# Kernel tuning notes

Hardware: AMD Instinct MI355X
Metric: run time of the kernel (lower is better)

Reference implementation:

```python
import jax, jax.numpy as jnp
import numpy as np

# Model/config dims
U, B, D, H, R, S, M = 512, 16, 512, 8, 32, 16, 32
HD = D // H
Q = R + U + S          # query length
KV = M + R + U         # key/value length
PE = 2 * U - 1         # relative position embedding length (training mode)
NEG_INF = -1e8
SCALE = HD ** -0.5


def setup_inputs() -> dict:
    key = jax.random.key(0)
    ks = jax.random.split(key, 14)
    f = lambda k, shp: jax.random.normal(k, shp, dtype=jnp.float32)
    return {
        "utterance": f(ks[0], (U, B, D)),
        "lengths": jax.random.randint(ks[1], (B,), U // 2, U + 1),
        "right_context": f(ks[2], (R, B, D)),
        "summary": f(ks[3], (S, B, D)),
        "memory": f(ks[4], (M, B, D)),
        "attention_mask": jax.random.bernoulli(ks[5], 0.5, (Q, KV)),  # True = masked
        "pos_emb": f(ks[6], (PE, D)),
        "Wq": f(ks[7], (D, D)) * 0.02, "bq": jnp.zeros((D,), jnp.float32),
        "Wkv": f(ks[8], (2 * D, D)) * 0.02, "bkv": jnp.zeros((2 * D,), jnp.float32),
        "Wo": f(ks[9], (D, D)) * 0.02, "bo": jnp.zeros((D,), jnp.float32),
        "Wpos": f(ks[10], (D, D)) * 0.02,
        "pos_bias_u": f(ks[11], (H, HD)) * 0.02,
        "pos_bias_v": f(ks[12], (H, HD)) * 0.02,
    }


def _rel_shift(x):
    # x: (B, H, U, PE) -> (B, H, U, PE - U + 1); out[..., u, j] = x[..., u, (U-1) - u + j]
    b, h, u, pe = x.shape
    out_len = pe - (u - 1)
    idx = (u - 1) - jnp.arange(u)[:, None] + jnp.arange(out_len)[None, :]  # (U, out_len)
    return jnp.take_along_axis(x, idx[None, None], axis=3)


def reference(utterance, lengths, right_context, summary, memory, attention_mask,
              pos_emb, Wq, bq, Wkv, bkv, Wo, bo, Wpos, pos_bias_u, pos_bias_v):
    # Projections
    query = jnp.concatenate([right_context, utterance, summary]) @ Wq.T + bq      # (Q, B, D)
    kv = jnp.concatenate([memory, right_context, utterance]) @ Wkv.T + bkv        # (KV, B, 2D)
    key_t, val_t = jnp.split(kv, 2, axis=2)                                       # (KV, B, D) each

    rk = key_t.reshape(KV, B * H, HD).transpose(1, 0, 2)                          # (B*H, KV, HD)
    rv = val_t.reshape(KV, B * H, HD).transpose(1, 0, 2)
    q4 = query.reshape(Q, B, H, HD)

    # content term (matrix AC) with pos_bias_u
    qu = (q4 + pos_bias_u).reshape(Q, B * H, HD).transpose(1, 0, 2)               # (B*H, Q, HD)
    matrix_ac = jnp.einsum('nqd,nkd->nqk', qu, rk)                                # (B*H, Q, KV)

    # positional term (matrix BD) with pos_bias_v, only for utterance queries
    uv = (q4[R:R + U] + pos_bias_v).transpose(1, 2, 0, 3)                         # (B, H, U, HD)
    pos = (pos_emb @ Wpos.T).reshape(PE, H, HD).transpose(1, 0, 2)                # (H, PE, HD)
    bd = jnp.einsum('bhud,hpd->bhup', uv, pos)                                    # (B, H, U, PE)
    bd = _rel_shift(bd).reshape(B * H, U, -1)                                     # (B*H, U, U)
    matrix_bd = jnp.zeros_like(matrix_ac).at[:, R:R + U, M + R:].set(bd)

    w = (matrix_ac + matrix_bd) * SCALE
    w = jnp.where(attention_mask[None], NEG_INF, w)
    # padding mask (B > 1 branch): pad positions where kv index >= KV - U + lengths
    pad = jnp.arange(KV)[None, :] >= (KV - U + lengths)[:, None]                  # (B, KV)
    w = jnp.where(pad[:, None, None, :], NEG_INF, w.reshape(B, H, Q, KV)).reshape(B * H, Q, KV)

    probs = jax.nn.softmax(w, axis=-1)
    attn = jnp.einsum('nqk,nkd->nqd', probs, rv)                                  # (B*H, Q, HD)
    attn = attn.transpose(1, 0, 2).reshape(Q, B, D)
    outputs = attn @ Wo.T + bo

    out_right_context_utterance = outputs[:R + U]                                 # (R+U, B, D)
    out_memory = jnp.clip(outputs[R + U:], -10.0, 10.0)                           # (S, B, D), tanh_on_mem=False
    return out_right_context_utterance, out_memory, key_t, val_t
```

## Files before the change

kernel.cpp:

```cpp
#include <hip/hip_runtime.h>
#include <math.h>


#define NEG_INF_F (-100000000.0f)
#define SCALE_F   (0.125f)

typedef short  short8 __attribute__((ext_vector_type(8)));
typedef float  f32x4  __attribute__((ext_vector_type(4)));
typedef unsigned short u16x4 __attribute__((ext_vector_type(4)));
typedef unsigned short u16x8 __attribute__((ext_vector_type(8)));

__device__ __forceinline__ unsigned short f2b(float f) {
    unsigned int u = __builtin_bit_cast(unsigned int, f);
    u = u + 0x7FFFu + ((u >> 16) & 1u);
    return (unsigned short)(u >> 16);
}
__device__ __forceinline__ float b2f(unsigned short h) {
    unsigned int u = ((unsigned int)h) << 16;
    return __builtin_bit_cast(float, u);
}

__device__ __forceinline__ int swzK(int row, int colB) {
    return row * 64 + ((colB ^ ((row & 7) << 4)) >> 1);
}
__device__ __forceinline__ int swzS(int row, int colB) {
    return row * 576 + ((colB ^ ((row & 7) << 4)) >> 1);
}

__global__ __launch_bounds__(256) void detect_mask_kernel(
    const unsigned int* __restrict__ m, int nwords, int* __restrict__ flags) {
    __shared__ int fF, fG;
    if (threadIdx.x == 0) { fF = 0; fG = 0; }
    __syncthreads();
    int lF = 0, lG = 0;
    for (int i = blockIdx.x * 256 + threadIdx.x; i < nwords; i += gridDim.x * 256) {
        unsigned int w = m[i];
        if (w == 0x3F800000u)      lF = 1;
        else if (w > 1u)           lG = 1;
    }
    if (lF) atomicOr(&fF, 1);
    if (lG) atomicOr(&fG, 1);
    __syncthreads();
    if (threadIdx.x == 0) {
        if (fF) atomicOr(&flags[0], 1);
        if (fG) atomicOr(&flags[1], 1);
    }
}

__global__ __launch_bounds__(256) void maskprep_kernel(
    const void* __restrict__ maskPtr, const int* __restrict__ flags,
    const int* __restrict__ lengths,
    unsigned short* __restrict__ maskBias, unsigned short* __restrict__ padBias)
{
    const int mode = flags[0] ? 2 : (flags[1] ? 1 : 0);
    const unsigned short NB = f2b(NEG_INF_F);
    for (int i = blockIdx.x * 256 + threadIdx.x; i < 560 * 576; i += gridDim.x * 256) {
        bool m;
        if (mode == 1)      m = ((const unsigned char*)maskPtr)[i] != 0;
        else if (mode == 2) m = ((const float*)maskPtr)[i] != 0.f;
        else                m = ((const int*)maskPtr)[i] != 0;
        maskBias[i] = m ? NB : (unsigned short)0;
    }
    for (int i = blockIdx.x * 256 + threadIdx.x; i < 16 * 576; i += gridDim.x * 256) {
        int b = i / 576, k = i - b * 576;
        padBias[i] = (k >= 64 + lengths[b]) ? NB : (unsigned short)0;
    }
}

__global__ __launch_bounds__(256) void conv9_kernel(
    const float* s0, const float* s1, const float* s2, const float* s3,
    const float* s4, const float* s5, const float* s6, const float* s7,
    const float* s8,
    unsigned short* d0, unsigned short* d1, unsigned short* d2,
    unsigned short* d3, unsigned short* d4, unsigned short* d5,
    unsigned short* d6, unsigned short* d7, unsigned short* d8,
    int n0, int n1, int n2, int n3, int n4, int n5, int n6, int n7, int n8)
{
    const float* ss[9] = {s0, s1, s2, s3, s4, s5, s6, s7, s8};
    unsigned short* dd[9] = {d0, d1, d2, d3, d4, d5, d6, d7, d8};
    int nn[9] = {n0, n1, n2, n3, n4, n5, n6, n7, n8};
    const int a = blockIdx.y;
    const float* s = ss[a];
    unsigned short* d = dd[a];
    const int nq = nn[a] >> 2;
    for (int i = blockIdx.x * 256 + threadIdx.x; i < nq; i += gridDim.x * 256) {
        float4 v = *(const float4*)(s + (size_t)i * 4);
        u16x4 o = {f2b(v.x), f2b(v.y), f2b(v.z), f2b(v.w)};
        *(u16x4*)(d + (size_t)i * 4) = o;
    }
}

struct GemmJob {
    const unsigned short *a0, *a1, *a2;
    int rb1, rb2, Mrows;
    const unsigned short *Wt;
    const float *bias;
    float *out0, *out1;
    unsigned short *auxU, *auxV;
    const float *pbu, *pbv;
    int mode, clampStart;
    int nBlocks;
    int base;
};

__global__ __launch_bounds__(256) void gemm_mfma3(GemmJob J0, GemmJob J1, GemmJob J2)
{
    __shared__ __attribute__((aligned(16))) unsigned short As[128 * 64];
    __shared__ __attribute__((aligned(16))) unsigned short Ws[128 * 64];

    const int bid = blockIdx.x;
    GemmJob J;
    if (bid >= J2.base)      J = J2;
    else if (bid >= J1.base) J = J1;
    else                     J = J0;
    const int rel = bid - J.base;
    const int bn = (rel % J.nBlocks) * 128;
    const int bm = (rel / J.nBlocks) * 128;

    const int tid = threadIdx.x;
    const int w = tid >> 6, lane = tid & 63;
    const int l15 = lane & 15, l4 = lane >> 4;
    const int wm = (w & 1) * 64, wn = (w >> 1) * 64;

    const int lrow  = lane >> 3;
    const int lslot = lane & 7;
    const int swzS16 = (lslot ^ lrow) * 8;

    const unsigned short* srcA[4];
    const unsigned short* srcW[4];
    #pragma unroll
    for (int c = 0; c < 4; ++c) {
        const int row = w * 32 + c * 8 + lrow;
        const int r = bm + row;
        const unsigned short* s;
        if (r < J.rb1)      s = J.a0 + (size_t)r * 512;
        else if (r < J.rb2) s = J.a1 + (size_t)(r - J.rb1) * 512;
        else                s = J.a2 + (size_t)(r - J.rb2) * 512;
        srcA[c] = s + swzS16;
        srcW[c] = J.Wt + (size_t)(bn + row) * 512 + swzS16;
    }

    f32x4 acc[4][4];
    #pragma unroll
    for (int i = 0; i < 4; ++i)
        #pragma unroll
        for (int j = 0; j < 4; ++j) acc[i][j] = (f32x4){0.f, 0.f, 0.f, 0.f};

    #define GFRAG(arr, row, kk) \
        (*(const short8*)&arr[(row) * 64 + ((((kk) * 4 + l4) ^ ((row) & 7)) * 8)])

    for (int kt = 0; kt < 8; ++kt) {
        __syncthreads();
        #pragma unroll
        for (int c = 0; c < 4; ++c) {
            __builtin_amdgcn_global_load_lds(
                (const __attribute__((address_space(1))) unsigned int*)(srcA[c] + kt * 64),
                (__attribute__((address_space(3))) unsigned int*)&As[(w * 32 + c * 8) * 64],
                16, 0, 0);
            __builtin_amdgcn_global_load_lds(
                (const __attribute__((address_space(1))) unsigned int*)(srcW[c] + kt * 64),
                (__attribute__((address_space(3))) unsigned int*)&Ws[(w * 32 + c * 8) * 64],
                16, 0, 0);
        }
        __syncthreads();

        short8 bfr[4][2];
        #pragma unroll
        for (int t = 0; t < 4; ++t) {
            const int r = wn + t * 16 + l15;
            bfr[t][0] = GFRAG(Ws, r, 0);
            bfr[t][1] = GFRAG(Ws, r, 1);
        }
        #pragma unroll
        for (int tm = 0; tm < 4; ++tm) {
            const int r = wm + tm * 16 + l15;
            const short8 a0f = GFRAG(As, r, 0);
            const short8 a1f = GFRAG(As, r, 1);
            #pragma unroll
            for (int tn = 0; tn < 4; ++tn) {
                acc[tm][tn] = __builtin_amdgcn_mfma_f32_16x16x32_bf16(
                    a0f, bfr[tn][0], acc[tm][tn], 0, 0, 0);
                acc[tm][tn] = __builtin_amdgcn_mfma_f32_16x16x32_bf16(
                    a1f, bfr[tn][1], acc[tm][tn], 0, 0, 0);
            }
        }
    }
    #undef GFRAG

    #pragma unroll
    for (int tm = 0; tm < 4; ++tm) {
        #pragma unroll
        for (int tn = 0; tn < 4; ++tn) {
            const int col = bn + wn + tn * 16 + l15;
            const float bv = J.bias ? J.bias[col] : 0.f;
            #pragma unroll
            for (int rr = 0; rr < 4; ++rr) {
                const int row = bm + wm + tm * 16 + l4 * 4 + rr;
                if (row >= J.Mrows) continue;
                float v = acc[tm][tn][rr] + bv;
                if (J.mode == 0) {
                    if (row >= J.clampStart) v = fminf(fmaxf(v, -10.f), 10.f);
                    J.out0[(size_t)row * 512 + col] = v;
                } else if (J.mode == 1) {
                    int bb = row & 15, kv = row >> 4;
                    if (col < 512) {
                        J.out0[(size_t)row * 512 + col] = v;
                        int hh = col >> 6, hd = col & 63;
                        J.auxU[(((size_t)(bb * 8 + hh)) * 576 + kv) * 64 + hd] = f2b(v);
                    } else {
                        J.out1[(size_t)row * 512 + (col - 512)] = v;
                        int cc = col - 512, hh = cc >> 6, hd = cc & 63;
                        J.auxV[(((size_t)(bb * 8 + hh)) * 64 + hd) * 576 + kv] = f2b(v);
                    }
                } else if (J.mode == 2) {
                    int q = row >> 4, bb = row & 15, hh = col >> 6, hd = col & 63;
                    size_t base = (((size_t)(bb * 8 + hh)) * 576 + q) * 64 + hd;
                    J.auxU[base] = f2b((v + J.pbu[col]) * SCALE_F);
                    J.auxV[base] = f2b((v + J.pbv[col]) * SCALE_F);
                } else {
                    int hh = col >> 6, hd = col & 63;
                    J.auxU[((size_t)hh * 1023 + row) * 64 + hd] = f2b(v);
                }
            }
        }
    }
}

__global__ __launch_bounds__(256) void attn_mfma_kernel(
    const unsigned short* __restrict__ Qu_g,
    const unsigned short* __restrict__ Qv_g,
    const unsigned short* __restrict__ K_g,
    const unsigned short* __restrict__ VT_g,
    const unsigned short* __restrict__ P_g,
    const unsigned short* __restrict__ maskBias,
    const unsigned short* __restrict__ padBias,
    unsigned short* __restrict__ attnT)
{
    __shared__ __attribute__((aligned(16))) unsigned short sc[32 * 576];
    __shared__ __attribute__((aligned(16))) unsigned short stg[2 * 4096];
    __shared__ float rowv[32];

    const int bid = blockIdx.y * 18 + blockIdx.x;
    const int workid = (bid & 7) * 288 + (bid >> 3);
    const int n = workid / 18;
    const int qt = workid - n * 18;

    const int b = n >> 3, h = n & 7;
    const int q0 = qt * 32;
    const int tid = threadIdx.x;
    const int w = tid >> 6, lane = tid & 63;
    const int l15 = lane & 15, l4 = lane >> 4;
    const int mT = (w >> 1) * 16;
    const int c0 = (w & 1) * 32;
    const int t0base = 16 - mT + c0;
    const bool hasBand = (qt >= 1 && qt <= 16);
    const int pbq = 512 - q0;

    const unsigned short* Kn  = K_g  + (size_t)n * 576 * 64;
    const unsigned short* VTn = VT_g + (size_t)n * 64 * 576;
    const unsigned short* Ph  = P_g  + (size_t)h * 1023 * 64;

    const int srow  = tid >> 3;
    const int sIdx  = (tid & 7) * 8;
    const int scolB = sIdx * 2;

    {
        u16x8 a = *(const u16x8*)&Kn[(size_t)srow * 64 + sIdx];
        u16x8 c = *(const u16x8*)&Kn[(size_t)(srow + 32) * 64 + sIdx];
        *(u16x8*)&stg[swzK(srow, scolB)] = a;
        *(u16x8*)&stg[swzK(srow + 32, scolB)] = c;
    }

    short8 quf[2], qvf[2];
    {
        size_t rb = ((size_t)n * 576 + q0 + mT + l15) * 64;
        quf[0] = *(const short8*)&Qu_g[rb + l4 * 8];
        quf[1] = *(const short8*)&Qu_g[rb + 32 + l4 * 8];
        qvf[0] = *(const short8*)&Qv_g[rb + l4 * 8];
        qvf[1] = *(const short8*)&Qv_g[rb + 32 + l4 * 8];
    }

    int cur = 0;
    for (int kt = 0; kt < 9; ++kt) {
        u16x8 kna, knb;
        if (kt < 8) {
            kna = *(const u16x8*)&Kn[(size_t)((kt + 1) * 64 + srow) * 64 + sIdx];
            knb = *(const u16x8*)&Kn[(size_t)((kt + 1) * 64 + srow + 32) * 64 + sIdx];
        }
        const bool doBand = hasBand && (kt >= 1);
        short8 bnd00, bnd01, bnd10, bnd11, bnd20, bnd21;
        if (doBand) {
            const int pbase = pbq + (kt - 1) * 64 + t0base + l15;
            int p0 = pbase;       p0 = p0 < 0 ? 0 : (p0 > 1022 ? 1022 : p0);
            int p1 = pbase + 16;  p1 = p1 < 0 ? 0 : (p1 > 1022 ? 1022 : p1);
            int p2 = pbase + 32;  p2 = p2 < 0 ? 0 : (p2 > 1022 ? 1022 : p2);
            bnd00 = *(const short8*)&Ph[(size_t)p0 * 64 + l4 * 8];
            bnd01 = *(const short8*)&Ph[(size_t)p0 * 64 + 32 + l4 * 8];
            bnd10 = *(const short8*)&Ph[(size_t)p1 * 64 + l4 * 8];
            bnd11 = *(const short8*)&Ph[(size_t)p1 * 64 + 32 + l4 * 8];
            bnd20 = *(const short8*)&Ph[(size_t)p2 * 64 + l4 * 8];
            bnd21 = *(const short8*)&Ph[(size_t)p2 * 64 + 32 + l4 * 8];
        }
        __syncthreads();
        unsigned short* buf = stg + cur * 4096;
        __builtin_amdgcn_s_setprio(1);
        #pragma unroll
        for (int s = 0; s < 2; ++s) {
            const int n0 = c0 + s * 16;
            f32x4 acc = {0.f, 0.f, 0.f, 0.f};
            short8 b0 = *(const short8*)&buf[swzK(n0 + l15, l4 * 16)];
            short8 b1 = *(const short8*)&buf[swzK(n0 + l15, 64 + l4 * 16)];
            acc = __builtin_amdgcn_mfma_f32_16x16x32_bf16(quf[0], b0, acc, 0, 0, 0);
            acc = __builtin_amdgcn_mfma_f32_16x16x32_bf16(quf[1], b1, acc, 0, 0, 0);
            const int col = kt * 64 + n0 + l15;
            #pragma unroll
            for (int r = 0; r < 4; ++r)
                sc[swzS(mT + l4 * 4 + r, col * 2)] = f2b(acc[r]);
        }
        __builtin_amdgcn_s_setprio(0);
        if (doBand) {
            #pragma unroll
            for (int s = 0; s < 3; ++s) {
                short8 ba = (s == 0) ? bnd00 : ((s == 1) ? bnd10 : bnd20);
                short8 bb = (s == 0) ? bnd01 : ((s == 1) ? bnd11 : bnd21);
                f32x4 acc = {0.f, 0.f, 0.f, 0.f};
                acc = __builtin_amdgcn_mfma_f32_16x16x32_bf16(qvf[0], ba, acc, 0, 0, 0);
                acc = __builtin_amdgcn_mfma_f32_16x16x32_bf16(qvf[1], bb, acc, 0, 0, 0);
                const int tl = t0base + s * 16 + l15;
                #pragma unroll
                for (int r = 0; r < 4; ++r) {
                    const int du = mT + l4 * 4 + r;
                    const int dj = tl - 31 + du;
                    if (dj >= c0 && dj < c0 + 32) {
                        const int ix = swzS(du, (kt * 64 + dj) * 2);
                        sc[ix] = f2b(b2f(sc[ix]) + acc[r]);
                    }
                }
            }
        }
        if (kt < 8) {
            unsigned short* nb = stg + (cur ^ 1) * 4096;
            *(u16x8*)&nb[swzK(srow, scolB)] = kna;
            *(u16x8*)&nb[swzK(srow + 32, scolB)] = knb;
        }
        cur ^= 1;
    }

    u16x8 va = *(const u16x8*)&VTn[(size_t)srow * 576 + sIdx];
    u16x8 vb = *(const u16x8*)&VTn[(size_t)(srow + 32) * 576 + sIdx];
    __syncthreads();

    {
        const int row = tid >> 3, seg = tid & 7;
        const int q = q0 + row;
        const int qc = q < 560 ? q : 559;
        const unsigned short* mb  = maskBias + (size_t)qc * 576 + seg * 72;
        const unsigned short* pbb = padBias + (size_t)b * 576 + seg * 72;
        float mx = -3.0e38f;
        #pragma unroll
        for (int ci = 0; ci < 9; ++ci) {
            u16x8 sv = *(const u16x8*)&sc[swzS(row, seg * 144 + ci * 16)];
            u16x8 mv = *(const u16x8*)&mb[ci * 8];
            u16x8 pv = *(const u16x8*)&pbb[ci * 8];
            #pragma unroll
            for (int j = 0; j < 8; ++j)
                mx = fmaxf(mx, b2f(sv[j]) + b2f(mv[j]) + b2f(pv[j]));
        }
        mx = fmaxf(mx, __shfl_xor(mx, 1));
        mx = fmaxf(mx, __shfl_xor(mx, 2));
        mx = fmaxf(mx, __shfl_xor(mx, 4));
        float lsum = 0.f;
        #pragma unroll
        for (int ci = 0; ci < 9; ++ci) {
            const int ix = swzS(row, seg * 144 + ci * 16);
            u16x8 sv = *(const u16x8*)&sc[ix];
            u16x8 mv = *(const u16x8*)&mb[ci * 8];
            u16x8 pv = *(const u16x8*)&pbb[ci * 8];
            u16x8 ev;
            #pragma unroll
            for (int j = 0; j < 8; ++j) {
                float e = __expf(b2f(sv[j]) + b2f(mv[j]) + b2f(pv[j]) - mx);
                ev[j] = f2b(e); lsum += e;
            }
            *(u16x8*)&sc[ix] = ev;
        }
        lsum += __shfl_xor(lsum, 1);
        lsum += __shfl_xor(lsum, 2);
        lsum += __shfl_xor(lsum, 4);
        if (seg == 0) rowv[row] = 1.f / lsum;
    }
    *(u16x8*)&stg[swzK(srow, scolB)] = va;
    *(u16x8*)&stg[swzK(srow + 32, scolB)] = vb;

    f32x4 oacc0 = {0.f, 0.f, 0.f, 0.f}, oacc1 = {0.f, 0.f, 0.f, 0.f};
    cur = 0;
    for (int kt = 0; kt < 9; ++kt) {
        u16x8 vna, vnb;
        if (kt < 8) {
            vna = *(const u16x8*)&VTn[(size_t)srow * 576 + (kt + 1) * 64 + sIdx];
            vnb = *(const u16x8*)&VTn[(size_t)(srow + 32) * 576 + (kt + 1) * 64 + sIdx];
        }
        __syncthreads();
        unsigned short* buf = stg + cur * 4096;
        short8 af0 = *(const short8*)&sc[swzS(mT + l15, kt * 128 + l4 * 16)];
        short8 af1 = *(const short8*)&sc[swzS(mT + l15, kt * 128 + 64 + l4 * 16)];
        __builtin_amdgcn_s_setprio(1);
        {
            short8 b00 = *(const short8*)&buf[swzK(c0 + l15, l4 * 16)];
            short8 b01 = *(const short8*)&buf[swzK(c0 + l15, 64 + l4 * 16)];
            short8 b10 = *(const short8*)&buf[swzK(c0 + 16 + l15, l4 * 16)];
            short8 b11 = *(const short8*)&buf[swzK(c0 + 16 + l15, 64 + l4 * 16)];
            oacc0 = __builtin_amdgcn_mfma_f32_16x16x32_bf16(af0, b00, oacc0, 0, 0, 0);
            oacc0 = __builtin_amdgcn_mfma_f32_16x16x32_bf16(af1, b01, oacc0, 0, 0, 0);
            oacc1 = __builtin_amdgcn_mfma_f32_16x16x32_bf16(af0, b10, oacc1, 0, 0, 0);
            oacc1 = __builtin_amdgcn_mfma_f32_16x16x32_bf16(af1, b11, oacc1, 0, 0, 0);
        }
        __builtin_amdgcn_s_setprio(0);
        if (kt < 8) {
            unsigned short* nb = stg + (cur ^ 1) * 4096;
            *(u16x8*)&nb[swzK(srow, scolB)] = vna;
            *(u16x8*)&nb[swzK(srow + 32, scolB)] = vnb;
        }
        cur ^= 1;
    }

    #pragma unroll
    for (int s = 0; s < 2; ++s) {
        const f32x4 oa = s ? oacc1 : oacc0;
        const int n0 = c0 + s * 16;
        #pragma unroll
        for (int r = 0; r < 4; ++r) {
            const int row = mT + l4 * 4 + r, q = q0 + row;
            if (q < 560)
                attnT[((size_t)q * 16 + b) * 512 + h * 64 + n0 + l15] =
                    f2b(oa[r] * rowv[row]);
        }
    }
}

extern "C" void kernel_launch(void* const* d_in, const int* in_sizes, int n_in,
                              void* d_out, int out_size, void* d_ws, size_t ws_size,
                              hipStream_t stream) {
    const float* utt     = (const float*)d_in[0];
    const int*   lengths = (const int*)d_in[1];
    const float* rc      = (const float*)d_in[2];
    const float* summ    = (const float*)d_in[3];
    const float* mem     = (const float*)d_in[4];
    const void*  mask    = d_in[5];
    const float* pos_emb = (const float*)d_in[6];
    const float* Wq      = (const float*)d_in[7];
    const float* bq      = (const float*)d_in[8];
    const float* Wkv     = (const float*)d_in[9];
    const float* bkv     = (const float*)d_in[10];
    const float* Wo      = (const float*)d_in[11];
    const float* bo      = (const float*)d_in[12];
    const float* Wpos    = (const float*)d_in[13];
    const float* pbu     = (const float*)d_in[14];
    const float* pbv     = (const float*)d_in[15];

    float* out = (float*)d_out;
    float* out0   = out;
    float* keyOut = out + 4587520;
    float* valOut = out + 9306112;

    int* flags = (int*)d_ws;
    unsigned short* U = (unsigned short*)d_ws + 64;
    unsigned short* utt_bf  = U;
    unsigned short* rc_bf   = utt_bf  + 4194304;
    unsigned short* summ_bf = rc_bf   + 262144;
    unsigned short* mem_bf  = summ_bf + 131072;
    unsigned short* pose_bf = mem_bf  + 262144;
    unsigned short* wq_bf   = pose_bf + 523776;
    unsigned short* wkv_bf  = wq_bf   + 262144;
    unsigned short* wo_bf   = wkv_bf  + 524288;
    unsigned short* wpos_bf = wo_bf   + 262144;
    unsigned short* Qu_bf   = wpos_bf + 262144;
    unsigned short* Qv_bf   = Qu_bf   + 4718592;
    unsigned short* K_bf    = Qv_bf   + 4718592;
    unsigned short* VT_bf   = K_bf    + 4718592;
    unsigned short* posW_bf = VT_bf   + 4718592;
    unsigned short* attnT_bf= posW_bf + 523776;
    unsigned short* maskB   = attnT_bf + 4587520;
    unsigned short* padB    = maskB + 322560;

    hipMemsetAsync(flags, 0, 2 * sizeof(int), stream);
    detect_mask_kernel<<<158, 256, 0, stream>>>((const unsigned int*)mask,
                                                (560 * 576) / 4, flags);
    maskprep_kernel<<<315, 256, 0, stream>>>(mask, flags, lengths, maskB, padB);

    conv9_kernel<<<dim3(1024, 9), 256, 0, stream>>>(
        utt, rc, summ, mem, pos_emb, Wq, Wkv, Wo, Wpos,
        utt_bf, rc_bf, summ_bf, mem_bf, pose_bf, wq_bf, wkv_bf, wo_bf, wpos_bf,
        4194304, 262144, 131072, 262144, 523776, 262144, 524288, 262144, 262144);

    GemmJob jq;
    jq.a0 = rc_bf; jq.a1 = utt_bf; jq.a2 = summ_bf;
    jq.rb1 = 512; jq.rb2 = 8704; jq.Mrows = 8960;
    jq.Wt = wq_bf; jq.bias = bq;
    jq.out0 = nullptr; jq.out1 = nullptr;
    jq.auxU = Qu_bf; jq.auxV = Qv_bf;
    jq.pbu = pbu; jq.pbv = pbv;
    jq.mode = 2; jq.clampStart = 0; jq.nBlocks = 4; jq.base = 0;

    GemmJob jkv;
    jkv.a0 = mem_bf; jkv.a1 = rc_bf; jkv.a2 = utt_bf;
    jkv.rb1 = 512; jkv.rb2 = 1024; jkv.Mrows = 9216;
    jkv.Wt = wkv_bf; jkv.bias = bkv;
    jkv.out0 = keyOut; jkv.out1 = valOut;
    jkv.auxU = K_bf; jkv.auxV = VT_bf;
    jkv.pbu = nullptr; jkv.pbv = nullptr;
    jkv.mode = 1; jkv.clampStart = 0; jkv.nBlocks = 8; jkv.base = 280;

    GemmJob jp;
    jp.a0 = pose_bf; jp.a1 = pose_bf; jp.a2 = pose_bf;
    jp.rb1 = 1 << 30; jp.rb2 = 1 << 30; jp.Mrows = 1023;
    jp.Wt = wpos_bf; jp.bias = nullptr;
    jp.out0 = nullptr; jp.out1 = nullptr;
    jp.auxU = posW_bf; jp.auxV = nullptr;
    jp.pbu = nullptr; jp.pbv = nullptr;
    jp.mode = 3; jp.clampStart = 0; jp.nBlocks = 4; jp.base = 856;

    gemm_mfma3<<<888, 256, 0, stream>>>(jq, jkv, jp);

    attn_mfma_kernel<<<dim3(18, 128), 256, 0, stream>>>(
        Qu_bf, Qv_bf, K_bf, VT_bf, posW_bf, maskB, padB, attnT_bf);

    GemmJob jo;
    jo.a0 = attnT_bf; jo.a1 = attnT_bf; jo.a2 = attnT_bf;
    jo.rb1 = 1 << 30; jo.rb2 = 1 << 30; jo.Mrows = 8960;
    jo.Wt = wo_bf; jo.bias = bo;
    jo.out0 = out0; jo.out1 = nullptr;
    jo.auxU = nullptr; jo.auxV = nullptr;
    jo.pbu = nullptr; jo.pbv = nullptr;
    jo.mode = 0; jo.clampStart = 8704; jo.nBlocks = 4; jo.base = 0;

    GemmJob jdummy = jo;
    jdummy.base = 1 << 30;

    gemm_mfma3<<<280, 256, 0, stream>>>(jo, jdummy, jdummy);
}
```

Baseline: 303.8 us.

## Fold mask kernels into convert/GEMM launches, use exp2 softmax, lighter barriers

Removes the separate mask-detect and mask-prep launches: mask detection becomes an extra blockIdx.y slice of the conversion kernel, and mask-bias preparation runs in 64 extra blocks appended to the projection GEMM grid. Queries are pre-scaled by log2(e) so the softmax can use the raw v_exp_f32 instruction instead of __expf. Some __syncthreads calls in the attention kernel are replaced with an inline-asm barrier that waits only on LDS counters. This saves two kernel launches and some ALU work, but if the barrier does not also wait on outstanding global loads, synchronization could be subtly wrong.

After: 303.3 us. About the same (-0.1%).

```diff
diff --git a/kernel.cpp b/kernel.cpp
--- a/kernel.cpp
+++ b/kernel.cpp
@@ -4,6 +4,7 @@
 
 #define NEG_INF_F (-100000000.0f)
 #define SCALE_F   (0.125f)
+#define LOG2E_F   (1.44269504f)
 
 typedef short  short8 __attribute__((ext_vector_type(8)));
 typedef float  f32x4  __attribute__((ext_vector_type(4)));
@@ -20,51 +21,21 @@
     return __builtin_bit_cast(float, u);
 }
 
+__device__ __forceinline__ float exp2_fast(float x) {
+    float r;
+    asm("v_exp_f32 %0, %1" : "=v"(r) : "v"(x));
+    return r;
+}
+
+__device__ __forceinline__ void barrier_lg() {
+    asm volatile("s_waitcnt lgkmcnt(0)\n\ts_barrier" ::: "memory");
+}
+
 __device__ __forceinline__ int swzK(int row, int colB) {
     return row * 64 + ((colB ^ ((row & 7) << 4)) >> 1);
 }
 __device__ __forceinline__ int swzS(int row, int colB) {
     return row * 576 + ((colB ^ ((row & 7) << 4)) >> 1);
-}
-
-__global__ __launch_bounds__(256) void detect_mask_kernel(
-    const unsigned int* __restrict__ m, int nwords, int* __restrict__ flags) {
-    __shared__ int fF, fG;
-    if (threadIdx.x == 0) { fF = 0; fG = 0; }
-    __syncthreads();
-    int lF = 0, lG = 0;
-    for (int i = blockIdx.x * 256 + threadIdx.x; i < nwords; i += gridDim.x * 256) {
-        unsigned int w = m[i];
-        if (w == 0x3F800000u)      lF = 1;
-        else if (w > 1u)           lG = 1;
-    }
-    if (lF) atomicOr(&fF, 1);
-    if (lG) atomicOr(&fG, 1);
-    __syncthreads();
-    if (threadIdx.x == 0) {
-        if (fF) atomicOr(&flags[0], 1);
-        if (fG) atomicOr(&flags[1], 1);
-    }
-}
-
-__global__ __launch_bounds__(256) void maskprep_kernel(
-    const void* __restrict__ maskPtr, const int* __restrict__ flags,
-    const int* __restrict__ lengths,
-    unsigned short* __restrict__ maskBias, unsigned short* __restrict__ padBias)
-{
-    const int mode = flags[0] ? 2 : (flags[1] ? 1 : 0);
-    const unsigned short NB = f2b(NEG_INF_F);
-    for (int i = blockIdx.x * 256 + threadIdx.x; i < 560 * 576; i += gridDim.x * 256) {
-        bool m;
-        if (mode == 1)      m = ((const unsigned char*)maskPtr)[i] != 0;
-        else if (mode == 2) m = ((const float*)maskPtr)[i] != 0.f;
-        else                m = ((const int*)maskPtr)[i] != 0;
-        maskBias[i] = m ? NB : (unsigned short)0;
-    }
-    for (int i = blockIdx.x * 256 + threadIdx.x; i < 16 * 576; i += gridDim.x * 256) {
-        int b = i / 576, k = i - b * 576;
-        padBias[i] = (k >= 64 + lengths[b]) ? NB : (unsigned short)0;
-    }
 }
 
 __global__ __launch_bounds__(256) void conv9_kernel(
@@ -74,12 +45,32 @@
     unsigned short* d0, unsigned short* d1, unsigned short* d2,
     unsigned short* d3, unsigned short* d4, unsigned short* d5,
     unsigned short* d6, unsigned short* d7, unsigned short* d8,
-    int n0, int n1, int n2, int n3, int n4, int n5, int n6, int n7, int n8)
+    int n0, int n1, int n2, int n3, int n4, int n5, int n6, int n7, int n8,
+    const unsigned int* __restrict__ mask, int nwords, int* __restrict__ flags)
 {
+    __shared__ int fF, fG;
+    const int a = blockIdx.y;
+    if (a == 9) {
+        if (threadIdx.x == 0) { fF = 0; fG = 0; }
+        __syncthreads();
+        int lF = 0, lG = 0;
+        for (int i = blockIdx.x * 256 + threadIdx.x; i < nwords; i += gridDim.x * 256) {
+            unsigned int w = mask[i];
+            if (w == 0x3F800000u)      lF = 1;
+            else if (w > 1u)           lG = 1;
+        }
+        if (lF) atomicOr(&fF, 1);
+        if (lG) atomicOr(&fG, 1);
+        __syncthreads();
+        if (threadIdx.x == 0) {
+            if (fF) atomicOr(&flags[0], 1);
+            if (fG) atomicOr(&flags[1], 1);
+        }
+        return;
+    }
     const float* ss[9] = {s0, s1, s2, s3, s4, s5, s6, s7, s8};
     unsigned short* dd[9] = {d0, d1, d2, d3, d4, d5, d6, d7, d8};
     int nn[9] = {n0, n1, n2, n3, n4, n5, n6, n7, n8};
-    const int a = blockIdx.y;
     const float* s = ss[a];
     unsigned short* d = dd[a];
     const int nq = nn[a] >> 2;
@@ -103,12 +94,36 @@
     int base;
 };
 
-__global__ __launch_bounds__(256) void gemm_mfma3(GemmJob J0, GemmJob J1, GemmJob J2)
+__global__ __launch_bounds__(256) void gemm_mfma3(
+    GemmJob J0, GemmJob J1, GemmJob J2,
+    const void* __restrict__ maskPtr, const int* __restrict__ flags,
+    const int* __restrict__ lengths,
+    unsigned short* __restrict__ maskB, unsigned short* __restrict__ padB,
+    int maskBase)
 {
     __shared__ __attribute__((aligned(16))) unsigned short As[128 * 64];
     __shared__ __attribute__((aligned(16))) unsigned short Ws[128 * 64];
 
     const int bid = blockIdx.x;
+    if (bid >= maskBase) {
+        const int mode = flags[0] ? 2 : (flags[1] ? 1 : 0);
+        const unsigned short NB = f2b(NEG_INF_F);
+        const int nBlk = gridDim.x - maskBase;
+        const int stride = nBlk * 256;
+        for (int i = (bid - maskBase) * 256 + threadIdx.x; i < 560 * 576; i += stride) {
+            bool m;
+            if (mode == 1)      m = ((const unsigned char*)maskPtr)[i] != 0;
+            else if (mode == 2) m = ((const float*)maskPtr)[i] != 0.f;
+            else                m = ((const int*)maskPtr)[i] != 0;
+            maskB[i] = m ? NB : (unsigned short)0;
+        }
+        for (int i = (bid - maskBase) * 256 + threadIdx.x; i < 16 * 576; i += stride) {
+            int b = i / 576, k = i - b * 576;
+            padB[i] = (k >= 64 + lengths[b]) ? NB : (unsigned short)0;
+        }
+        return;
+    }
+
     GemmJob J;
     if (bid >= J2.base)      J = J2;
     else if (bid >= J1.base) J = J1;
@@ -215,8 +230,8 @@
                 } else if (J.mode == 2) {
                     int q = row >> 4, bb = row & 15, hh = col >> 6, hd = col & 63;
                     size_t base = (((size_t)(bb * 8 + hh)) * 576 + q) * 64 + hd;
-                    J.auxU[base] = f2b((v + J.pbu[col]) * SCALE_F);
-                    J.auxV[base] = f2b((v + J.pbv[col]) * SCALE_F);
+                    J.auxU[base] = f2b((v + J.pbu[col]) * (SCALE_F * LOG2E_F));
+                    J.auxV[base] = f2b((v + J.pbv[col]) * (SCALE_F * LOG2E_F));
                 } else {
                     int hh = col >> 6, hd = col & 63;
                     J.auxU[((size_t)hh * 1023 + row) * 64 + hd] = f2b(v);
@@ -301,7 +316,7 @@
             bnd20 = *(const short8*)&Ph[(size_t)p2 * 64 + l4 * 8];
             bnd21 = *(const short8*)&Ph[(size_t)p2 * 64 + 32 + l4 * 8];
         }
-        __syncthreads();
+        barrier_lg();
         unsigned short* buf = stg + cur * 4096;
         __builtin_amdgcn_s_setprio(1);
         #pragma unroll
@@ -348,7 +363,7 @@
 
     u16x8 va = *(const u16x8*)&VTn[(size_t)srow * 576 + sIdx];
     u16x8 vb = *(const u16x8*)&VTn[(size_t)(srow + 32) * 576 + sIdx];
-    __syncthreads();
+    barrier_lg();
 
     {
         const int row = tid >> 3, seg = tid & 7;
@@ -379,7 +394,7 @@
             u16x8 ev;
             #pragma unroll
             for (int j = 0; j < 8; ++j) {
-                float e = __expf(b2f(sv[j]) + b2f(mv[j]) + b2f(pv[j]) - mx);
+                float e = exp2_fast(b2f(sv[j]) + b2f(mv[j]) + b2f(pv[j]) - mx);
                 ev[j] = f2b(e); lsum += e;
             }
             *(u16x8*)&sc[ix] = ev;
@@ -400,7 +415,7 @@
             vna = *(const u16x8*)&VTn[(size_t)srow * 576 + (kt + 1) * 64 + sIdx];
             vnb = *(const u16x8*)&VTn[(size_t)(srow + 32) * 576 + (kt + 1) * 64 + sIdx];
         }
-        __syncthreads();
+        barrier_lg();
         unsigned short* buf = stg + cur * 4096;
         short8 af0 = *(const short8*)&sc[swzS(mT + l15, kt * 128 + l4 * 16)];
         short8 af1 = *(const short8*)&sc[swzS(mT + l15, kt * 128 + 64 + l4 * 16)];
@@ -483,15 +498,13 @@
     unsigned short* maskB   = attnT_bf + 4587520;
     unsigned short* padB    = maskB + 322560;
 
-    hipMemsetAsync(flags, 0, 2 * sizeof(int), stream);
-    detect_mask_kernel<<<158, 256, 0, stream>>>((const unsigned int*)mask,
-                                                (560 * 576) / 4, flags);
-    maskprep_kernel<<<315, 256, 0, stream>>>(mask, flags, lengths, maskB, padB);
-
-    conv9_kernel<<<dim3(1024, 9), 256, 0, stream>>>(
+    (void)hipMemsetAsync(flags, 0, 2 * sizeof(int), stream);
+
+    conv9_kernel<<<dim3(1024, 10), 256, 0, stream>>>(
         utt, rc, summ, mem, pos_emb, Wq, Wkv, Wo, Wpos,
         utt_bf, rc_bf, summ_bf, mem_bf, pose_bf, wq_bf, wkv_bf, wo_bf, wpos_bf,
-        4194304, 262144, 131072, 262144, 523776, 262144, 524288, 262144, 262144);
+        4194304, 262144, 131072, 262144, 523776, 262144, 524288, 262144, 262144,
+        (const unsigned int*)mask, (560 * 576) / 4, flags);
 
     GemmJob jq;
     jq.a0 = rc_bf; jq.a1 = utt_bf; jq.a2 = summ_bf;
@@ -520,7 +533,8 @@
     jp.pbu = nullptr; jp.pbv = nullptr;
     jp.mode = 3; jp.clampStart = 0; jp.nBlocks = 4; jp.base = 856;
 
-    gemm_mfma3<<<888, 256, 0, stream>>>(jq, jkv, jp);
+    gemm_mfma3<<<952, 256, 0, stream>>>(jq, jkv, jp,
+        mask, flags, lengths, maskB, padB, 888);
 
     attn_mfma_kernel<<<dim3(18, 128), 256, 0, stream>>>(
         Qu_bf, Qv_bf, K_bf, VT_bf, posW_bf, maskB, padB, attnT_bf);
@@ -537,5 +551,6 @@
     GemmJob jdummy = jo;
     jdummy.base = 1 << 30;
 
-    gemm_mfma3<<<280, 256, 0, stream>>>(jo, jdummy, jdummy);
-}
+    gemm_mfma3<<<280, 256, 0, stream>>>(jo, jdummy, jdummy,
+        mask, flags, lengths, maskB, padB, 1 << 30);
+}
```
